# Kernel tuning notes

Hardware: AMD Instinct MI355X
Metric: run time of the kernel (lower is better)

The kernel has to match this reference:

```python
import jax, jax.numpy as jnp
import numpy as np

N_NODES = 100000


def gcn_layer(x, W, b, src, dst, n):
    # add self loops
    loop = jnp.arange(n, dtype=src.dtype)
    s = jnp.concatenate([src, loop])
    d = jnp.concatenate([dst, loop])
    # degree computed over row (source) of edge_index with self loops,
    # matching PyG degree(row, size[0])
    deg = jax.ops.segment_sum(jnp.ones_like(s, dtype=x.dtype), s, num_segments=n)
    dinv = jax.lax.rsqrt(deg)  # self loops guarantee deg >= 1
    h = x @ W + b  # [n, out]
    norm = dinv[s] * dinv[d]  # [E+n]
    msg = norm[:, None] * h[s]  # gather from source nodes
    return jax.ops.segment_sum(msg, d, num_segments=n)  # scatter-add to targets


def setup_inputs() -> dict:
    key = jax.random.key(0)
    k1, k2, k3, k4 = jax.random.split(key, 4)
    nfeat, nhid, nclass = 512, 16, 40
    E = 3200000
    x = jax.random.normal(k1, (N_NODES, nfeat), dtype=jnp.float32)
    edge_index = jax.random.randint(k2, (2, E), 0, N_NODES, dtype=jnp.int64)
    W1 = jax.random.normal(k3, (nfeat, nhid), dtype=jnp.float32) * (1.0 / np.sqrt(nfeat))
    b1 = jnp.zeros((nhid,), dtype=jnp.float32)
    W2 = jax.random.normal(k4, (nhid, nclass), dtype=jnp.float32) * (1.0 / np.sqrt(nhid))
    b2 = jnp.zeros((nclass,), dtype=jnp.float32)
    return {"x": x, "edge_index": edge_index, "W1": W1, "b1": b1, "W2": W2, "b2": b2}


def reference(x, edge_index, W1, b1, W2, b2):
    n = x.shape[0]
    src, dst = edge_index[0], edge_index[1]
    h = gcn_layer(x, W1, b1, src, dst, n)
    h = jax.nn.relu(h)
    # dropout: eval mode (identity), matching F.dropout(training=False)
    h = gcn_layer(h, W2, b2, src, dst, n)
    return jax.nn.log_softmax(h, axis=1)
```

## Files before the change

kernel.cpp:

```cpp
#include <hip/hip_runtime.h>
#include <hip/hip_bf16.h>

#define BSH 9
#define BSZ 512
#define CAP 17408
#define CHK 4096

typedef __attribute__((ext_vector_type(8))) short bf16x8;
typedef __attribute__((ext_vector_type(4))) float f32x4;

__device__ __forceinline__ unsigned short f2bf(float f) {
    unsigned u = __float_as_uint(f);
    u += 0x7fffu + ((u >> 16) & 1u);
    return (unsigned short)(u >> 16);
}
__device__ __forceinline__ float b2f(unsigned short v) {
    return __uint_as_float((unsigned)v << 16);
}

__global__ void init_k(int* __restrict__ curD, int* __restrict__ curS, int nbk) {
    int i = threadIdx.x;
    if (i < nbk) { curD[i] = i * CAP; curS[i] = i * CAP; }
}


#define GROWS 64
#define GKC 256
#define GSTR 264

__global__ __launch_bounds__(256) void fused_gs_k(
    const float* __restrict__ X, const float* __restrict__ W, const float* __restrict__ B,
    float* __restrict__ H, int n, int nGm,
    const int* __restrict__ src, const int* __restrict__ dst, int E,
    int* __restrict__ curD, int* __restrict__ curS,
    unsigned int* __restrict__ pairs, unsigned short* __restrict__ sbuf, int nbk) {
    __shared__ char smem[GROWS * GSTR * 2];
    int t = threadIdx.x;

    if ((int)blockIdx.x < nGm) {
        unsigned short* xt = (unsigned short*)smem;
        int lane = t & 63, wave = t >> 6;
        int rowBase = blockIdx.x * GROWS;
        int bn = lane & 15;

        {
            int kt0 = t >> 4, kg0 = (t >> 2) & 3, bn0 = (t & 3) * 4;
            unsigned short frag[4][8];
#pragma unroll
            for (int j = 0; j < 8; ++j) {
                float4 w = *(const float4*)&W[(size_t)(kt0 * 32 + kg0 * 8 + j) * 16 + bn0];
                frag[0][j] = f2bf(w.x); frag[1][j] = f2bf(w.y);
                frag[2][j] = f2bf(w.z); frag[3][j] = f2bf(w.w);
            }
#pragma unroll
            for (int b = 0; b < 4; ++b)
                *(uint4*)&xt[((kt0 * 4 + kg0) * 16 + bn0 + b) * 8] = *(const uint4*)frag[b];
        }
        __syncthreads();
        bf16x8 bw[16];
#pragma unroll
        for (int kt = 0; kt < 16; ++kt)
            bw[kt] = *(const bf16x8*)&xt[(kt * 64 + lane) * 8];
        float bias = B[bn];
        __syncthreads();

        f32x4 acc = {0.f, 0.f, 0.f, 0.f};
        int srow = t >> 4, skq = t & 15;

        for (int ch = 0; ch < 2; ++ch) {
#pragma unroll
            for (int p = 0; p < 4; ++p) {
                int r = p * 16 + srow;
                int gr = rowBase + r;
                const float* xr = &X[(size_t)(gr < n ? gr : n - 1) * 512 + ch * GKC + skq * 4];
#pragma unroll
                for (int q = 0; q < 4; ++q) {
                    float4 v = *(const float4*)&xr[q * 64];
                    ushort4 u;
                    u.x = f2bf(v.x); u.y = f2bf(v.y); u.z = f2bf(v.z); u.w = f2bf(v.w);
                    *(ushort4*)&xt[r * GSTR + skq * 4 + q * 64] = u;
                }
            }
            __syncthreads();

            int rb = (wave * 16 + bn) * GSTR + (lane >> 4) * 8;
#pragma unroll
            for (int kt = 0; kt < 8; ++kt) {
                bf16x8 af = *(const bf16x8*)&xt[rb + kt * 32];
                acc = __builtin_amdgcn_mfma_f32_16x16x32_bf16(af, bw[ch * 8 + kt], acc, 0, 0, 0);
            }
            __syncthreads();
        }

        int r0 = rowBase + wave * 16 + (lane >> 4) * 4;
#pragma unroll
        for (int i = 0; i < 4; ++i) {
            int row = r0 + i;
            if (row < n) H[(size_t)row * 16 + bn] = acc[i] + bias;
        }
    } else {
        unsigned int*   stageD = (unsigned int*)smem;
        unsigned short* stageS = (unsigned short*)(smem + 16384);
        int* cntD  = (int*)(smem + 24576);
        int* cntS  = (int*)(smem + 25600);
        int* rsvD  = (int*)(smem + 26624);
        int* rsvS  = (int*)(smem + 27648);
        int* scanD = (int*)(smem + 28672);
        int* scanS = (int*)(smem + 29696);
        int* ps    = (int*)(smem + 30720);

        int bb = blockIdx.x - nGm;
        int lo = bb * CHK, hi = min(E, lo + CHK);
        bool full = (hi - lo) == CHK;

        cntD[t] = 0; cntS[t] = 0;
        __syncthreads();

        int sv[16], dv[16];
        if (full) {
#pragma unroll
            for (int j = 0; j < 16; j++) {
                int i = lo + t + j * 256;
                sv[j] = src[i]; dv[j] = dst[i];
            }
#pragma unroll
            for (int j = 0; j < 16; j++) {
                atomicAdd(&cntD[dv[j] >> BSH], 1);
                atomicAdd(&cntS[sv[j] >> BSH], 1);
            }
        } else {
            for (int i = lo + t; i < hi; i += 256) {
                atomicAdd(&cntD[dst[i] >> BSH], 1);
                atomicAdd(&cntS[src[i] >> BSH], 1);
            }
        }
        __syncthreads();
        int vD = cntD[t];
        ps[t] = vD; __syncthreads();
        for (int o = 1; o < 256; o <<= 1) {
            int u = (t >= o) ? ps[t - o] : 0; __syncthreads();
            ps[t] += u; __syncthreads();
        }
        scanD[t] = ps[t] - vD;
        if (t < nbk && vD) rsvD[t] = atomicAdd(&curD[t], vD);
        __syncthreads();
        int vS = cntS[t];
        ps[t] = vS; __syncthreads();
        for (int o = 1; o < 256; o <<= 1) {
            int u = (t >= o) ? ps[t - o] : 0; __syncthreads();
            ps[t] += u; __syncthreads();
        }
        scanS[t] = ps[t] - vS;
        if (t < nbk && vS) rsvS[t] = atomicAdd(&curS[t], vS);
        cntD[t] = 0; cntS[t] = 0;
        __syncthreads();
        if (full) {
#pragma unroll
            for (int j = 0; j < 16; j++) {
                int s = sv[j], d = dv[j];
                int bd = d >> BSH;
                int pd = scanD[bd] + atomicAdd(&cntD[bd], 1);
                stageD[pd] = ((unsigned int)s << BSH) | (unsigned int)(d & (BSZ - 1));
                int bs = s >> BSH;
                int pp = scanS[bs] + atomicAdd(&cntS[bs], 1);
                stageS[pp] = (unsigned short)(s & (BSZ - 1));
            }
        } else {
            for (int i = lo + t; i < hi; i += 256) {
                int s = src[i], d = dst[i];
                int bd = d >> BSH;
                int pd = scanD[bd] + atomicAdd(&cntD[bd], 1);
                stageD[pd] = ((unsigned int)s << BSH) | (unsigned int)(d & (BSZ - 1));
                int bs = s >> BSH;
                int pp = scanS[bs] + atomicAdd(&cntS[bs], 1);
                stageS[pp] = (unsigned short)(s & (BSZ - 1));
            }
        }
        __syncthreads();
        int wave = t >> 6, lane = t & 63;
        for (int b = wave; b < nbk; b += 4) {
            int st = scanD[b], len = cntD[b], g = rsvD[b];
            for (int j = lane; j < len; j += 64) pairs[g + j] = stageD[st + j];
        }
        for (int b = wave; b < nbk; b += 4) {
            int st = scanS[b], len = cntS[b], g = rsvS[b];
            for (int j = lane; j < len; j += 64) sbuf[g + j] = stageS[st + j];
        }
    }
}


__global__ __launch_bounds__(256) void dinvScale_k(const unsigned short* __restrict__ sbuf,
                                                   const int* __restrict__ curS,
                                                   const float* __restrict__ h1,
                                                   float* __restrict__ dinv,
                                                   unsigned short* __restrict__ hw1, int n) {
    __shared__ int cnt[BSZ];
    __shared__ float dl[BSZ];
    int b = blockIdx.x, t = threadIdx.x;
    cnt[t] = 0; cnt[t + 256] = 0;
    __syncthreads();
    int lo = b * CAP, hi = curS[b];
    for (int i = lo + t; i < hi; i += 256) atomicAdd(&cnt[sbuf[i]], 1);
    __syncthreads();
    int n0 = b * BSZ + t, n1 = n0 + 256;
    float d0 = rsqrtf((float)(1 + cnt[t]));
    float d1 = rsqrtf((float)(1 + cnt[t + 256]));
    dl[t] = d0; dl[t + 256] = d1;
    if (n0 < n) dinv[n0] = d0;
    if (n1 < n) dinv[n1] = d1;
    __syncthreads();
    int rows = min(BSZ, n - b * BSZ);
    int lim4 = rows * 4;
    size_t base = (size_t)b * BSZ * 16;
#pragma unroll
    for (int j = 0; j < 8; j++) {
        int i4 = j * 256 + t;
        if (i4 < lim4) {
            float4 v = *(const float4*)&h1[base + (size_t)i4 * 4];
            float d = dl[i4 >> 2];
            ushort4 u;
            u.x = f2bf(v.x * d); u.y = f2bf(v.y * d);
            u.z = f2bf(v.z * d); u.w = f2bf(v.w * d);
            *(ushort4*)&hw1[base + (size_t)i4 * 4] = u;
        }
    }
}


#define FPS 65536.f
#define FPI (1.f / 65536.f)

template <int LAYER>
__global__ __launch_bounds__(1024) void aggB_k(
    const unsigned int* __restrict__ pairs, const int* __restrict__ curD,
    const unsigned short* __restrict__ HW, const float* __restrict__ dinv,
    float* __restrict__ rowsum, const float* __restrict__ W2,
    const float* __restrict__ B2, unsigned short* __restrict__ outA,
    float* __restrict__ outF, int n, int nc) {
    __shared__ int iacc[BSZ * 16];
    __shared__ unsigned int rsl[BSZ];
    int b = blockIdx.x, t = threadIdx.x;
    for (int i = t; i < BSZ * 16; i += 1024) iacc[i] = 0;
    if (LAYER == 1)
        for (int i = t; i < BSZ; i += 1024) rsl[i] = 0u;
    __syncthreads();

    int lo = b * CAP, hi = curD[b];
    int q = t & 3;
    int i = lo + (t >> 2);
    for (; i + 256 < hi; i += 512) {
        unsigned int p0 = pairs[i], p1 = pairs[i + 256];
        int s0 = p0 >> BSH, l0 = p0 & (BSZ - 1);
        int s1 = p1 >> BSH, l1 = p1 & (BSZ - 1);
        ushort4 u0 = *(const ushort4*)&HW[(size_t)s0 * 16 + q * 4];
        ushort4 u1 = *(const ushort4*)&HW[(size_t)s1 * 16 + q * 4];
        int* a0 = &iacc[l0 * 16 + q * 4];
        atomicAdd(&a0[0], __float2int_rn(b2f(u0.x) * FPS));
        atomicAdd(&a0[1], __float2int_rn(b2f(u0.y) * FPS));
        atomicAdd(&a0[2], __float2int_rn(b2f(u0.z) * FPS));
        atomicAdd(&a0[3], __float2int_rn(b2f(u0.w) * FPS));
        int* a1 = &iacc[l1 * 16 + q * 4];
        atomicAdd(&a1[0], __float2int_rn(b2f(u1.x) * FPS));
        atomicAdd(&a1[1], __float2int_rn(b2f(u1.y) * FPS));
        atomicAdd(&a1[2], __float2int_rn(b2f(u1.z) * FPS));
        atomicAdd(&a1[3], __float2int_rn(b2f(u1.w) * FPS));
        if (LAYER == 1 && q == 0) {
            atomicAdd(&rsl[l0], (unsigned int)(dinv[s0] * FPS + 0.5f));
            atomicAdd(&rsl[l1], (unsigned int)(dinv[s1] * FPS + 0.5f));
        }
    }
    if (i < hi) {
        unsigned int p0 = pairs[i];
        int s0 = p0 >> BSH, l0 = p0 & (BSZ - 1);
        ushort4 u0 = *(const ushort4*)&HW[(size_t)s0 * 16 + q * 4];
        int* a0 = &iacc[l0 * 16 + q * 4];
        atomicAdd(&a0[0], __float2int_rn(b2f(u0.x) * FPS));
        atomicAdd(&a0[1], __float2int_rn(b2f(u0.y) * FPS));
        atomicAdd(&a0[2], __float2int_rn(b2f(u0.z) * FPS));
        atomicAdd(&a0[3], __float2int_rn(b2f(u0.w) * FPS));
        if (LAYER == 1 && q == 0) atomicAdd(&rsl[l0], (unsigned int)(dinv[s0] * FPS + 0.5f));
    }
    __syncthreads();

    if (LAYER == 1) {
        int ln = t >> 1, f0 = (t & 1) * 8;
        int node = b * BSZ + ln;
        if (node < n) {
            float dd = dinv[node];
            const ushort4* sp = (const ushort4*)&HW[(size_t)node * 16 + f0];
            ushort4 s0 = sp[0], s1 = sp[1];
            const int* ap = &iacc[ln * 16 + f0];
            ushort4 o0, o1;
            o0.x = f2bf(dd * fmaxf(dd * ((float)ap[0] * FPI + b2f(s0.x)), 0.f));
            o0.y = f2bf(dd * fmaxf(dd * ((float)ap[1] * FPI + b2f(s0.y)), 0.f));
            o0.z = f2bf(dd * fmaxf(dd * ((float)ap[2] * FPI + b2f(s0.z)), 0.f));
            o0.w = f2bf(dd * fmaxf(dd * ((float)ap[3] * FPI + b2f(s0.w)), 0.f));
            o1.x = f2bf(dd * fmaxf(dd * ((float)ap[4] * FPI + b2f(s1.x)), 0.f));
            o1.y = f2bf(dd * fmaxf(dd * ((float)ap[5] * FPI + b2f(s1.y)), 0.f));
            o1.z = f2bf(dd * fmaxf(dd * ((float)ap[6] * FPI + b2f(s1.z)), 0.f));
            o1.w = f2bf(dd * fmaxf(dd * ((float)ap[7] * FPI + b2f(s1.w)), 0.f));
            ushort4* op = (ushort4*)&outA[(size_t)node * 16 + f0];
            op[0] = o0; op[1] = o1;
            if (f0 == 0) rowsum[node] = dd * (dd + (float)rsl[ln] * FPI);
        }
    } else {
        int wave = t >> 6, lane = t & 63;
        int node0 = b * BSZ;
        int nodeEnd = min(node0 + BSZ, n);
        for (int node = node0 + wave; node < nodeEnd; node += 16) {
            int ln = node - node0;
            float dd = dinv[node];
            float f[16];
            const ushort4* sp = (const ushort4*)&HW[(size_t)node * 16];
#pragma unroll
            for (int g = 0; g < 4; g++) {
                ushort4 u = sp[g];
                f[g * 4 + 0] = dd * ((float)iacc[ln * 16 + g * 4 + 0] * FPI + b2f(u.x));
                f[g * 4 + 1] = dd * ((float)iacc[ln * 16 + g * 4 + 1] * FPI + b2f(u.y));
                f[g * 4 + 2] = dd * ((float)iacc[ln * 16 + g * 4 + 2] * FPI + b2f(u.z));
                f[g * 4 + 3] = dd * ((float)iacc[ln * 16 + g * 4 + 3] * FPI + b2f(u.w));
            }
            float logit = -1e30f;
            if (lane < nc) {
                logit = rowsum[node] * B2[lane];
#pragma unroll
                for (int k = 0; k < 16; k++) logit = fmaf(f[k], W2[k * nc + lane], logit);
            }
            float m = logit;
#pragma unroll
            for (int off = 1; off < 64; off <<= 1) m = fmaxf(m, __shfl_xor(m, off, 64));
            float e = (lane < nc) ? __expf(logit - m) : 0.f;
            float s = e;
#pragma unroll
            for (int off = 1; off < 64; off <<= 1) s += __shfl_xor(s, off, 64);
            if (lane < nc) outF[(size_t)node * nc + lane] = logit - m - __logf(s);
        }
    }
}


extern "C" void kernel_launch(void* const* d_in, const int* in_sizes, int n_in,
                              void* d_out, int out_size, void* d_ws, size_t ws_size,
                              hipStream_t stream) {
    const float* X  = (const float*)d_in[0];
    const int*   EI = (const int*)d_in[1];
    const float* W1 = (const float*)d_in[2];
    const float* B1 = (const float*)d_in[3];
    const float* W2 = (const float*)d_in[4];
    const float* B2 = (const float*)d_in[5];
    float* out = (float*)d_out;

    int NH = in_sizes[3];
    int NC = in_sizes[5];
    int NF = in_sizes[2] / NH;
    int n  = in_sizes[0] / NF;
    int E  = in_sizes[1] / 2;
    const int* src = EI;
    const int* dst = EI + E;
    int nbk = (n + BSZ - 1) >> BSH;

    char* ws = (char*)d_ws;
    size_t o = 0;
    auto alloc = [&](size_t bytes) { size_t r = o; o = (o + bytes + 255) & ~(size_t)255; return r; };
    size_t o_dinv   = alloc((size_t)n * 4);
    size_t o_rsum   = alloc((size_t)n * 4);
    size_t o_curD   = alloc(1024);
    size_t o_curS   = alloc(1024);
    size_t o_pairs  = alloc((size_t)nbk * CAP * 4);
    size_t o_sbuf   = alloc((size_t)nbk * CAP * 2);
    size_t o_h1     = alloc((size_t)n * 16 * 4);
    size_t o_hw1    = alloc((size_t)n * 16 * 2);
    size_t o_a1w    = alloc((size_t)n * 16 * 2);

    float* dinv  = (float*)(ws + o_dinv);
    float* rsum  = (float*)(ws + o_rsum);
    int* curD    = (int*)(ws + o_curD);
    int* curS    = (int*)(ws + o_curS);
    unsigned int* pairs   = (unsigned int*)(ws + o_pairs);
    unsigned short* sbuf  = (unsigned short*)(ws + o_sbuf);
    float* h1    = (float*)(ws + o_h1);
    unsigned short* hw1 = (unsigned short*)(ws + o_hw1);
    unsigned short* a1w = (unsigned short*)(ws + o_a1w);

    init_k<<<1, 256, 0, stream>>>(curD, curS, nbk);

    int NBLK = (E + CHK - 1) / CHK;
    int nGm = (n + GROWS - 1) / GROWS;
    fused_gs_k<<<nGm + NBLK, 256, 0, stream>>>(X, W1, B1, h1, n, nGm,
                                               src, dst, E, curD, curS,
                                               pairs, sbuf, nbk);
    dinvScale_k<<<nbk, 256, 0, stream>>>(sbuf, curS, h1, dinv, hw1, n);

    aggB_k<1><<<nbk, 1024, 0, stream>>>(pairs, curD, hw1, dinv, rsum,
                                        nullptr, nullptr, a1w, nullptr, n, NC);
    aggB_k<2><<<nbk, 1024, 0, stream>>>(pairs, curD, a1w, dinv, rsum,
                                        W2, B2, nullptr, out, n, NC);
}
```

Before: 207.2 us.

## Split each aggregation bucket across four blocks by destination quarter

Result: slower. 433.4 us (+109.2%).

```diff
diff --git a/kernel.cpp b/kernel.cpp
--- a/kernel.cpp
+++ b/kernel.cpp
@@ -230,6 +230,7 @@
 
 #define FPS 65536.f
 #define FPI (1.f / 65536.f)
+#define QN 128
 
 template <int LAYER>
 __global__ __launch_bounds__(1024) void aggB_k(
@@ -238,76 +239,62 @@
     float* __restrict__ rowsum, const float* __restrict__ W2,
     const float* __restrict__ B2, unsigned short* __restrict__ outA,
     float* __restrict__ outF, int n, int nc) {
-    __shared__ int iacc[BSZ * 16];
-    __shared__ unsigned int rsl[BSZ];
-    int b = blockIdx.x, t = threadIdx.x;
-    for (int i = t; i < BSZ * 16; i += 1024) iacc[i] = 0;
-    if (LAYER == 1)
-        for (int i = t; i < BSZ; i += 1024) rsl[i] = 0u;
+    __shared__ int iacc[QN * 16];
+    __shared__ unsigned int rsl[QN];
+    int bq = blockIdx.x;
+    int b = bq >> 2, qi = bq & 3;
+    int t = threadIdx.x;
+    for (int i = t; i < QN * 16; i += 1024) iacc[i] = 0;
+    if (LAYER == 1 && t < QN) rsl[t] = 0u;
     __syncthreads();
 
     int lo = b * CAP, hi = curD[b];
     int q = t & 3;
-    int i = lo + (t >> 2);
-    for (; i + 256 < hi; i += 512) {
-        unsigned int p0 = pairs[i], p1 = pairs[i + 256];
-        int s0 = p0 >> BSH, l0 = p0 & (BSZ - 1);
-        int s1 = p1 >> BSH, l1 = p1 & (BSZ - 1);
-        ushort4 u0 = *(const ushort4*)&HW[(size_t)s0 * 16 + q * 4];
-        ushort4 u1 = *(const ushort4*)&HW[(size_t)s1 * 16 + q * 4];
-        int* a0 = &iacc[l0 * 16 + q * 4];
-        atomicAdd(&a0[0], __float2int_rn(b2f(u0.x) * FPS));
-        atomicAdd(&a0[1], __float2int_rn(b2f(u0.y) * FPS));
-        atomicAdd(&a0[2], __float2int_rn(b2f(u0.z) * FPS));
-        atomicAdd(&a0[3], __float2int_rn(b2f(u0.w) * FPS));
-        int* a1 = &iacc[l1 * 16 + q * 4];
-        atomicAdd(&a1[0], __float2int_rn(b2f(u1.x) * FPS));
-        atomicAdd(&a1[1], __float2int_rn(b2f(u1.y) * FPS));
-        atomicAdd(&a1[2], __float2int_rn(b2f(u1.z) * FPS));
-        atomicAdd(&a1[3], __float2int_rn(b2f(u1.w) * FPS));
-        if (LAYER == 1 && q == 0) {
-            atomicAdd(&rsl[l0], (unsigned int)(dinv[s0] * FPS + 0.5f));
-            atomicAdd(&rsl[l1], (unsigned int)(dinv[s1] * FPS + 0.5f));
+    int lbase = qi * QN;
+    for (int i = lo + (t >> 2); i < hi; i += 256) {
+        unsigned int p0 = pairs[i];
+        int l0 = p0 & (BSZ - 1);
+        if ((l0 >> 7) == qi) {
+            int s0 = p0 >> BSH;
+            ushort4 u0 = *(const ushort4*)&HW[(size_t)s0 * 16 + q * 4];
+            int* a0 = &iacc[(l0 - lbase) * 16 + q * 4];
+            atomicAdd(&a0[0], __float2int_rn(b2f(u0.x) * FPS));
+            atomicAdd(&a0[1], __float2int_rn(b2f(u0.y) * FPS));
+            atomicAdd(&a0[2], __float2int_rn(b2f(u0.z) * FPS));
+            atomicAdd(&a0[3], __float2int_rn(b2f(u0.w) * FPS));
+            if (LAYER == 1 && q == 0)
+                atomicAdd(&rsl[l0 - lbase], (unsigned int)(dinv[s0] * FPS + 0.5f));
         }
     }
-    if (i < hi) {
-        unsigned int p0 = pairs[i];
-        int s0 = p0 >> BSH, l0 = p0 & (BSZ - 1);
-        ushort4 u0 = *(const ushort4*)&HW[(size_t)s0 * 16 + q * 4];
-        int* a0 = &iacc[l0 * 16 + q * 4];
-        atomicAdd(&a0[0], __float2int_rn(b2f(u0.x) * FPS));
-        atomicAdd(&a0[1], __float2int_rn(b2f(u0.y) * FPS));
-        atomicAdd(&a0[2], __float2int_rn(b2f(u0.z) * FPS));
-        atomicAdd(&a0[3], __float2int_rn(b2f(u0.w) * FPS));
-        if (LAYER == 1 && q == 0) atomicAdd(&rsl[l0], (unsigned int)(dinv[s0] * FPS + 0.5f));
-    }
-    __syncthreads();
-
+    __syncthreads();
+
+    int node0 = b * BSZ + lbase;
     if (LAYER == 1) {
-        int ln = t >> 1, f0 = (t & 1) * 8;
-        int node = b * BSZ + ln;
-        if (node < n) {
-            float dd = dinv[node];
-            const ushort4* sp = (const ushort4*)&HW[(size_t)node * 16 + f0];
-            ushort4 s0 = sp[0], s1 = sp[1];
-            const int* ap = &iacc[ln * 16 + f0];
-            ushort4 o0, o1;
-            o0.x = f2bf(dd * fmaxf(dd * ((float)ap[0] * FPI + b2f(s0.x)), 0.f));
-            o0.y = f2bf(dd * fmaxf(dd * ((float)ap[1] * FPI + b2f(s0.y)), 0.f));
-            o0.z = f2bf(dd * fmaxf(dd * ((float)ap[2] * FPI + b2f(s0.z)), 0.f));
-            o0.w = f2bf(dd * fmaxf(dd * ((float)ap[3] * FPI + b2f(s0.w)), 0.f));
-            o1.x = f2bf(dd * fmaxf(dd * ((float)ap[4] * FPI + b2f(s1.x)), 0.f));
-            o1.y = f2bf(dd * fmaxf(dd * ((float)ap[5] * FPI + b2f(s1.y)), 0.f));
-            o1.z = f2bf(dd * fmaxf(dd * ((float)ap[6] * FPI + b2f(s1.z)), 0.f));
-            o1.w = f2bf(dd * fmaxf(dd * ((float)ap[7] * FPI + b2f(s1.w)), 0.f));
-            ushort4* op = (ushort4*)&outA[(size_t)node * 16 + f0];
-            op[0] = o0; op[1] = o1;
-            if (f0 == 0) rowsum[node] = dd * (dd + (float)rsl[ln] * FPI);
+        if (t < QN * 2) {
+            int ln = t >> 1, f0 = (t & 1) * 8;
+            int node = node0 + ln;
+            if (node < n) {
+                float dd = dinv[node];
+                const ushort4* sp = (const ushort4*)&HW[(size_t)node * 16 + f0];
+                ushort4 s0 = sp[0], s1 = sp[1];
+                const int* ap = &iacc[ln * 16 + f0];
+                ushort4 o0, o1;
+                o0.x = f2bf(dd * fmaxf(dd * ((float)ap[0] * FPI + b2f(s0.x)), 0.f));
+                o0.y = f2bf(dd * fmaxf(dd * ((float)ap[1] * FPI + b2f(s0.y)), 0.f));
+                o0.z = f2bf(dd * fmaxf(dd * ((float)ap[2] * FPI + b2f(s0.z)), 0.f));
+                o0.w = f2bf(dd * fmaxf(dd * ((float)ap[3] * FPI + b2f(s0.w)), 0.f));
+                o1.x = f2bf(dd * fmaxf(dd * ((float)ap[4] * FPI + b2f(s1.x)), 0.f));
+                o1.y = f2bf(dd * fmaxf(dd * ((float)ap[5] * FPI + b2f(s1.y)), 0.f));
+                o1.z = f2bf(dd * fmaxf(dd * ((float)ap[6] * FPI + b2f(s1.z)), 0.f));
+                o1.w = f2bf(dd * fmaxf(dd * ((float)ap[7] * FPI + b2f(s1.w)), 0.f));
+                ushort4* op = (ushort4*)&outA[(size_t)node * 16 + f0];
+                op[0] = o0; op[1] = o1;
+                if (f0 == 0) rowsum[node] = dd * (dd + (float)rsl[ln] * FPI);
+            }
         }
     } else {
         int wave = t >> 6, lane = t & 63;
-        int node0 = b * BSZ;
-        int nodeEnd = min(node0 + BSZ, n);
+        int nodeEnd = min(node0 + QN, n);
         for (int node = node0 + wave; node < nodeEnd; node += 16) {
             int ln = node - node0;
             float dd = dinv[node];
@@ -392,8 +379,8 @@
                                                pairs, sbuf, nbk);
     dinvScale_k<<<nbk, 256, 0, stream>>>(sbuf, curS, h1, dinv, hw1, n);
 
-    aggB_k<1><<<nbk, 1024, 0, stream>>>(pairs, curD, hw1, dinv, rsum,
-                                        nullptr, nullptr, a1w, nullptr, n, NC);
-    aggB_k<2><<<nbk, 1024, 0, stream>>>(pairs, curD, a1w, dinv, rsum,
-                                        W2, B2, nullptr, out, n, NC);
-}
+    aggB_k<1><<<nbk * 4, 1024, 0, stream>>>(pairs, curD, hw1, dinv, rsum,
+                                            nullptr, nullptr, a1w, nullptr, n, NC);
+    aggB_k<2><<<nbk * 4, 1024, 0, stream>>>(pairs, curD, a1w, dinv, rsum,
+                                            W2, B2, nullptr, out, n, NC);
+}
```
